# Performance work log

Hardware: AMD Instinct MI355X
Metric: run time of the kernel (lower is better)

The kernel has to match this reference:

```python
import jax, jax.numpy as jnp
import numpy as np
import math

N, E, MUL = 10000, 160000, 128
D = MUL * 4  # 128x0e (128) + 128x1o (384) = 512
NEURONS = 32
EDGE_ATTR_DIM = 32
WEIGHT_NUMEL = 4 * MUL  # 4 uvu tensor-product paths, 128 weights each


def ssp(x):
    return jax.nn.softplus(x) - math.log(2.0)


def irrep_linear(x, W0, b0, W1):
    # o3.Linear on 128x0e+128x1o: mixes mul channels within each irrep, fan-in normalized,
    # bias only on scalar (0e) block.
    s = x[:, :MUL] @ (W0 / jnp.sqrt(MUL)) + b0
    v = x[:, MUL:].reshape(-1, MUL, 3)
    v = jnp.einsum('num,uv->nvm', v, W1) / jnp.sqrt(MUL)
    return jnp.concatenate([s, v.reshape(-1, MUL * 3)], axis=-1)


def inner_product(a, b):
    # InnerProduct: uuu channel-wise irrep inner product, 1/sqrt(dim) normalized
    s = a[:, :MUL] * b[:, :MUL]
    va = a[:, MUL:].reshape(-1, MUL, 3)
    vb = b[:, MUL:].reshape(-1, MUL, 3)
    v = jnp.einsum('num,num->nu', va, vb) / jnp.sqrt(3.0)
    return jnp.concatenate([s, v], axis=-1)


def norm_gate(x, W1, b1, W2, b2):
    # NormGate: per-channel norms of l>0 irreps -> MLP gates -> gate l>0 channels
    v = x[:, MUL:].reshape(-1, MUL, 3)
    norm_v = jnp.sqrt(jnp.sum(v * v, axis=-1) + 1e-12)      # [n, 128]
    f0 = jnp.concatenate([x[:, :MUL], norm_v], axis=-1)     # [n, 256]
    g = jax.nn.silu(f0 @ W1 + b1) @ W2 + b2                 # [n, 256]
    gated = v * g[:, MUL:, None]
    return jnp.concatenate([g[:, :MUL], gated.reshape(-1, MUL * 3)], axis=-1)


def mlp2(x, Wa, Wb):
    # e3nn FullyConnectedNet: fan-in normalized, ssp nonlinearity on hidden layer only
    return ssp(x @ (Wa / jnp.sqrt(Wa.shape[0]))) @ (Wb / jnp.sqrt(Wb.shape[0]))


def setup_inputs():
    key = jax.random.key(0)
    ks = jax.random.split(key, 20)
    r = lambda i, shp: jax.random.normal(ks[i], shp, dtype=jnp.float32)
    return {
        'x': r(0, (N, D)),
        'edge_index': jax.random.randint(ks[1], (2, E), 0, N, dtype=jnp.int32),
        'edge_attr': jax.random.uniform(ks[2], (E, EDGE_ATTR_DIM), dtype=jnp.float32),
        'edge_sh': r(3, (E, 4)),
        'Wp0': r(4, (MUL, MUL)), 'bp0': jnp.zeros((MUL,), jnp.float32), 'Wp1': r(5, (MUL, MUL)),
        'ngW1': r(6, (2 * MUL, 2 * MUL)) / 16.0, 'ngb1': jnp.zeros((2 * MUL,), jnp.float32),
        'ngW2': r(7, (2 * MUL, 2 * MUL)) / 16.0, 'ngb2': jnp.zeros((2 * MUL,), jnp.float32),
        'Wn0': r(8, (MUL, MUL)), 'bn0': jnp.zeros((MUL,), jnp.float32), 'Wn1': r(9, (MUL, MUL)),
        'fcnW1': r(10, (EDGE_ATTR_DIM, NEURONS)), 'fcnW2': r(11, (NEURONS, WEIGHT_NUMEL)),
        'l0W1': r(12, (3 * MUL, NEURONS)), 'l0W2': r(13, (NEURONS, WEIGHT_NUMEL)),
        'Wo0': r(14, (MUL, MUL)), 'bo0': jnp.zeros((MUL,), jnp.float32), 'Wo1': r(15, (MUL, MUL)),
    }


def reference(x, edge_index, edge_attr, edge_sh, Wp0, bp0, Wp1, ngW1, ngb1, ngW2, ngb2,
              Wn0, bn0, Wn1, fcnW1, fcnW2, l0W1, l0W2, Wo0, bo0, Wo1):
    edge_dst, edge_src = edge_index[0], edge_index[1]
    # invariant edge descriptor s0 from pre-linear + inner product
    pre_x = irrep_linear(x, Wp0, bp0, Wp1)
    ip = inner_product(pre_x[edge_dst], pre_x[edge_src])[:, MUL:]             # [E,128]
    s0 = jnp.concatenate([pre_x[edge_dst][:, :MUL], pre_x[edge_src][:, :MUL], ip], axis=-1)  # [E,384]
    # norm-gate + linear on node features
    x = norm_gate(x, ngW1, ngb1, ngW2, ngb2)
    x = irrep_linear(x, Wn0, bn0, Wn1)
    self_x = x
    # per-edge tensor-product weights: fc_node(edge_attr) * layer_l0(s0)
    w = mlp2(edge_attr, fcnW1, fcnW2) * mlp2(s0, l0W1, l0W2)                   # [E,512]
    w1, w2, w3, w4 = w[:, :MUL], w[:, MUL:2 * MUL], w[:, 2 * MUL:3 * MUL], w[:, 3 * MUL:]
    xs = x[edge_src]
    xs0 = xs[:, :MUL]                     # [E,128]
    xs1 = xs[:, MUL:].reshape(E, MUL, 3)  # [E,128,3]
    sh0 = edge_sh[:, 0:1]
    sh1 = edge_sh[:, 1:4]
    # uvu CG tensor product paths: 0ex0e->0e, 0ex1o->1o, 1ox0e->1o, 1ox1o->0e
    c0, c1 = 0.5, jnp.sqrt(3.0) / 2.0  # path norm sqrt(ir_out.dim / n_paths)
    out0 = c0 * (w1 * xs0 * sh0 + w4 * jnp.einsum('eum,em->eu', xs1, sh1) / jnp.sqrt(3.0))
    out1 = c1 * (w2[:, :, None] * xs0[:, :, None] * sh1[:, None, :]
                 + w3[:, :, None] * xs1 * sh0[:, :, None])
    edge_feat = jnp.concatenate([out0, out1.reshape(E, MUL * 3)], axis=-1)     # [E,512]
    # scatter-aggregate to destination nodes, residual, output linear
    out = jax.ops.segment_sum(edge_feat, edge_dst, num_segments=N)
    out = out + self_x
    return irrep_linear(out, Wo0, bo0, Wo1)
```

## Files before the change

kernel.cpp:

```cpp
#include <hip/hip_runtime.h>
#include <hip/hip_fp16.h>
#include <math.h>

#define NN 10000
#define EE 160000
#define DPB 8

#define RS128 0.08838834764831845f
#define RS384 0.05103103630798287f
#define RS32  0.17677669529663687f
#define R3    0.57735026918962576f
#define C1V   0.86602540378443865f

typedef _Float16 half8 __attribute__((ext_vector_type(8)));
typedef _Float16 half4 __attribute__((ext_vector_type(4)));
typedef float f32x4 __attribute__((ext_vector_type(4)));

__device__ __forceinline__ float sspf(float x) {
    return fmaxf(x, 0.0f) + log1pf(__expf(-fabsf(x))) - 0.69314718055994530942f;
}

__device__ __forceinline__ void packone(const float* __restrict__ W,
                                        _Float16* __restrict__ P,
                                        int K, int N, int off) {
    const int KS = K >> 5;
    int j = off & 7, lane = (off >> 3) & 63, rest = off >> 9;
    int ks = rest % KS, ct = rest / KS;
    int k = ks * 32 + ((lane >> 4) << 3) + j;
    int c = ct * 16 + (lane & 15);
    P[off] = (_Float16)W[k * N + c];
}

__global__ __launch_bounds__(256) void k_packall(
    const float* __restrict__ Wp0, const float* __restrict__ Wp1,
    const float* __restrict__ Wn0, const float* __restrict__ Wn1,
    const float* __restrict__ Wo0, const float* __restrict__ Wo1,
    const float* __restrict__ ngW1, const float* __restrict__ ngW2,
    const float* __restrict__ l0W1, const float* __restrict__ fcnW1,
    const float* __restrict__ fcnW2, const float* __restrict__ l0W2,
    _Float16* __restrict__ pWp0, _Float16* __restrict__ pWp1,
    _Float16* __restrict__ pWn0, _Float16* __restrict__ pWn1,
    _Float16* __restrict__ pWo0, _Float16* __restrict__ pWo1,
    _Float16* __restrict__ png1, _Float16* __restrict__ png2,
    _Float16* __restrict__ pWc, _Float16* __restrict__ pWa,
    _Float16* __restrict__ Wf_t, _Float16* __restrict__ Wl_t) {
    int idx = blockIdx.x * 256 + threadIdx.x;
    if (idx < 98304) {
        int seg = idx >> 14, off = idx & 16383;
        if (seg == 0) packone(Wp0, pWp0, 128, 128, off);
        else if (seg == 1) packone(Wp1, pWp1, 128, 128, off);
        else if (seg == 2) packone(Wn0, pWn0, 128, 128, off);
        else if (seg == 3) packone(Wn1, pWn1, 128, 128, off);
        else if (seg == 4) packone(Wo0, pWo0, 128, 128, off);
        else packone(Wo1, pWo1, 128, 128, off);
    } else if (idx < 229376) {
        int r = idx - 98304;
        if (r < 65536) packone(ngW1, png1, 256, 256, r);
        else packone(ngW2, png2, 256, 256, r - 65536);
    } else if (idx < 233472) {
        packone(l0W1 + 256 * 32, pWc, 128, 32, idx - 229376);
    } else if (idx < 234496) {
        packone(fcnW1, pWa, 32, 32, idx - 233472);
    } else {
        int off = idx - 234496;
        int k = off & 31, c = off >> 5;
        Wf_t[c * 32 + k] = (_Float16)fcnW2[k * 512 + c];
        Wl_t[c * 32 + k] = (_Float16)l0W2[k * 512 + c];
    }
}

__global__ __launch_bounds__(256) void k_irrep_m(
    const float* __restrict__ X, const _Float16* __restrict__ pW0,
    const float* __restrict__ b0, const _Float16* __restrict__ pW1,
    float* __restrict__ out) {
    __shared__ _Float16 Xr[4][16][136];
    const int t = threadIdx.x, lane = t & 63, w = t >> 6;
    const int nb = blockIdx.x * 16;
    for (int idx = t; idx < 16 * 128; idx += 256) {
        int n = idx >> 7, c4 = idx & 127;
        const float4 v = *(const float4*)(X + (size_t)(nb + n) * 512 + 4 * c4);
        float vals[4] = {v.x, v.y, v.z, v.w};
        int c = 4 * c4;
#pragma unroll
        for (int j = 0; j < 4; ++j) {
            int cc = c + j;
            if (cc < 128) Xr[0][n][cc] = (_Float16)vals[j];
            else { int d = cc - 128; Xr[1 + d % 3][n][d / 3] = (_Float16)vals[j]; }
        }
    }
    __syncthreads();
    const _Float16* pW = (w == 0) ? pW0 : pW1;
    const int row16 = lane & 15, kg = lane >> 4;
    f32x4 acc[8];
    const f32x4 zero = {0.0f, 0.0f, 0.0f, 0.0f};
#pragma unroll
    for (int ct = 0; ct < 8; ++ct) acc[ct] = zero;
    for (int ks = 0; ks < 4; ++ks) {
        const half8 a = *(const half8*)&Xr[w][row16][ks * 32 + kg * 8];
#pragma unroll
        for (int ct = 0; ct < 8; ++ct) {
            const half8 b = *(const half8*)(pW + (((ct * 4 + ks) * 64 + lane) << 3));
            acc[ct] = __builtin_amdgcn_mfma_f32_16x16x32_f16(a, b, acc[ct], 0, 0, 0);
        }
    }
#pragma unroll
    for (int ct = 0; ct < 8; ++ct) {
        const int col = ct * 16 + row16;
        const float bb = (w == 0) ? b0[col] : 0.0f;
#pragma unroll
        for (int r = 0; r < 4; ++r) {
            const int node = nb + kg * 4 + r;
            const float val = acc[ct][r] * RS128 + bb;
            if (w == 0) out[(size_t)node * 512 + col] = val;
            else out[(size_t)node * 512 + 128 + 3 * col + (w - 1)] = val;
        }
    }
}

__global__ __launch_bounds__(256) void k_self_m(
    const float* __restrict__ X,
    const _Float16* __restrict__ png1, const float* __restrict__ ngb1,
    const _Float16* __restrict__ png2, const float* __restrict__ ngb2,
    const _Float16* __restrict__ pWn0, const float* __restrict__ bn0,
    const _Float16* __restrict__ pWn1,
    _Float16* __restrict__ selfx_h) {
    __shared__ _Float16 f0h[16][264];
    __shared__ _Float16 t1h[16][264];
    __shared__ _Float16 xvh[3][16][136];
    const int t = threadIdx.x, lane = t & 63, w = t >> 6;
    const int nb = blockIdx.x * 16;
    const int row16 = lane & 15, kg = lane >> 4;
    const f32x4 zero = {0.0f, 0.0f, 0.0f, 0.0f};

    for (int idx = t; idx < 16 * 128; idx += 256) {
        int n = idx >> 7, c4 = idx & 127;
        const float4 v = *(const float4*)(X + (size_t)(nb + n) * 512 + 4 * c4);
        float vals[4] = {v.x, v.y, v.z, v.w};
        int c = 4 * c4;
#pragma unroll
        for (int j = 0; j < 4; ++j) {
            int cc = c + j;
            if (cc < 128) f0h[n][cc] = (_Float16)vals[j];
            else { int d = cc - 128; xvh[d % 3][n][d / 3] = (_Float16)vals[j]; }
        }
    }
    __syncthreads();
    for (int idx = t; idx < 16 * 128; idx += 256) {
        int n = idx >> 7, u = idx & 127;
        float a = (float)xvh[0][n][u], b = (float)xvh[1][n][u], c = (float)xvh[2][n][u];
        f0h[n][128 + u] = (_Float16)sqrtf(fmaf(a, a, fmaf(b, b, fmaf(c, c, 1e-12f))));
    }
    __syncthreads();
    {
        f32x4 acc[4];
#pragma unroll
        for (int i = 0; i < 4; ++i) acc[i] = zero;
        for (int ks = 0; ks < 8; ++ks) {
            const half8 a = *(const half8*)&f0h[row16][ks * 32 + kg * 8];
#pragma unroll
            for (int c2 = 0; c2 < 4; ++c2) {
                const int ct = 4 * w + c2;
                const half8 b = *(const half8*)(png1 + (((ct * 8 + ks) * 64 + lane) << 3));
                acc[c2] = __builtin_amdgcn_mfma_f32_16x16x32_f16(a, b, acc[c2], 0, 0, 0);
            }
        }
#pragma unroll
        for (int c2 = 0; c2 < 4; ++c2) {
            const int col = (4 * w + c2) * 16 + row16;
            const float bb = ngb1[col];
#pragma unroll
            for (int r = 0; r < 4; ++r) {
                const float z = acc[c2][r] + bb;
                t1h[kg * 4 + r][col] = (_Float16)(z / (1.0f + __expf(-z)));
            }
        }
    }
    __syncthreads();
    {
        f32x4 acc[4];
#pragma unroll
        for (int i = 0; i < 4; ++i) acc[i] = zero;
        for (int ks = 0; ks < 8; ++ks) {
            const half8 a = *(const half8*)&t1h[row16][ks * 32 + kg * 8];
#pragma unroll
            for (int c2 = 0; c2 < 4; ++c2) {
                const int ct = 4 * w + c2;
                const half8 b = *(const half8*)(png2 + (((ct * 8 + ks) * 64 + lane) << 3));
                acc[c2] = __builtin_amdgcn_mfma_f32_16x16x32_f16(a, b, acc[c2], 0, 0, 0);
            }
        }
        __syncthreads();
#pragma unroll
        for (int c2 = 0; c2 < 4; ++c2) {
            const int col = (4 * w + c2) * 16 + row16;
            const float bb = ngb2[col];
#pragma unroll
            for (int r = 0; r < 4; ++r)
                f0h[kg * 4 + r][col] = (_Float16)(acc[c2][r] + bb);
        }
    }
    __syncthreads();
    for (int idx = t; idx < 16 * 128; idx += 256) {
        int n = idx >> 7, u = idx & 127;
        const _Float16 g = f0h[n][128 + u];
        xvh[0][n][u] = xvh[0][n][u] * g;
        xvh[1][n][u] = xvh[1][n][u] * g;
        xvh[2][n][u] = xvh[2][n][u] * g;
    }
    __syncthreads();
    {
        const _Float16* pw = (w == 0) ? pWn0 : pWn1;
        f32x4 acc[8];
#pragma unroll
        for (int ct = 0; ct < 8; ++ct) acc[ct] = zero;
        for (int ks = 0; ks < 4; ++ks) {
            const half8 a = (w == 0)
                ? *(const half8*)&f0h[row16][ks * 32 + kg * 8]
                : *(const half8*)&xvh[w - 1][row16][ks * 32 + kg * 8];
#pragma unroll
            for (int ct = 0; ct < 8; ++ct) {
                const half8 b = *(const half8*)(pw + (((ct * 4 + ks) * 64 + lane) << 3));
                acc[ct] = __builtin_amdgcn_mfma_f32_16x16x32_f16(a, b, acc[ct], 0, 0, 0);
            }
        }
#pragma unroll
        for (int ct = 0; ct < 8; ++ct) {
            const int col = ct * 16 + row16;
            const float bb = (w == 0) ? bn0[col] : 0.0f;
#pragma unroll
            for (int r = 0; r < 4; ++r) {
                const int n = kg * 4 + r;
                const float val = acc[ct][r] * RS128 + bb;
                if (w == 0) f0h[n][col] = (_Float16)val;
                else xvh[w - 1][n][col] = (_Float16)val;
            }
        }
    }
    __syncthreads();
    for (int idx = t; idx < 16 * 128; idx += 256) {
        int n = idx >> 7, u = idx & 127;
        half4 sx = {f0h[n][u], xvh[0][n][u], xvh[1][n][u], xvh[2][n][u]};
        *(half4*)(selfx_h + (size_t)(nb + n) * 512 + (u << 2)) = sx;
    }
}

__global__ __launch_bounds__(256) void k_pre(
    const float* __restrict__ prex, const float* __restrict__ l0W1,
    float* __restrict__ pAB) {
    __shared__ float xs[8][128];
    const int t = threadIdx.x;
    const int nb = blockIdx.x * 8;
    for (int idx = t; idx < 8 * 128; idx += 256) {
        int n = idx >> 7, u = idx & 127;
        xs[n][u] = prex[(size_t)(nb + n) * 512 + u];
    }
    __syncthreads();
    const int n = t >> 5, k = t & 31;
    float a = 0, b = 0;
    for (int u = 0; u < 128; ++u) {
        float s = xs[n][u];
        a = fmaf(s, l0W1[u * 32 + k], a);
        b = fmaf(s, l0W1[(128 + u) * 32 + k], b);
    }
    pAB[(size_t)(nb + n) * 64 + k] = a;
    pAB[(size_t)(nb + n) * 64 + 32 + k] = b;
}

__global__ __launch_bounds__(256) void k_deg(const int* __restrict__ ei, int* __restrict__ deg) {
    int e = blockIdx.x * 256 + threadIdx.x;
    if (e < EE) atomicAdd(&deg[ei[e]], 1);
}

__global__ __launch_bounds__(1024) void k_scan(const int* __restrict__ deg, int* __restrict__ row_ptr) {
    __shared__ int part[1024];
    const int t = threadIdx.x;
    const int base = t * 10;
    int loc[10];
    int s = 0;
#pragma unroll
    for (int i = 0; i < 10; ++i) {
        int idx = base + i;
        int d = (idx < NN) ? deg[idx] : 0;
        loc[i] = s;
        s += d;
    }
    part[t] = s;
    __syncthreads();
    for (int off = 1; off < 1024; off <<= 1) {
        int v = (t >= off) ? part[t - off] : 0;
        __syncthreads();
        part[t] += v;
        __syncthreads();
    }
    int excl = (t > 0) ? part[t - 1] : 0;
#pragma unroll
    for (int i = 0; i < 10; ++i) {
        int idx = base + i;
        if (idx <= NN) row_ptr[idx] = excl + loc[i];
    }
}

__global__ __launch_bounds__(256) void k_fill(const int* __restrict__ ei,
                                              const int* __restrict__ row_ptr,
                                              int* __restrict__ cursor,
                                              int* __restrict__ csr_eid) {
    int e = blockIdx.x * 256 + threadIdx.x;
    if (e < EE) {
        int d = ei[e];
        int pos = atomicAdd(&cursor[d], 1);
        csr_eid[row_ptr[d] + pos] = e;
    }
}

__global__ __launch_bounds__(256) void k_hidden_m(
    const float* __restrict__ prex, const float* __restrict__ pAB,
    const int* __restrict__ edge_index, const float* __restrict__ edge_attr,
    const int* __restrict__ csr_eid,
    const _Float16* __restrict__ pWc, const _Float16* __restrict__ pWa,
    __half* __restrict__ hh) {
    const int pb = blockIdx.x * 32;
    const int t = threadIdx.x, lane = t & 63, w = t >> 6;
    __shared__ _Float16 ipl[32][132];
    __shared__ _Float16 eal[32][36];
    __shared__ _Float16 h1o[32][32];
    __shared__ _Float16 hao[32][32];
    __shared__ int dsts[32], srcs[32], eids[32];

    if (t < 32) {
        const int id = csr_eid[pb + t];
        eids[t] = id;
        dsts[t] = edge_index[id];
        srcs[t] = edge_index[EE + id];
    }
    __syncthreads();
    for (int idx = t; idx < 32 * 32; idx += 256) {
        int e = idx >> 5, j = idx & 31;
        eal[e][j] = (_Float16)edge_attr[(size_t)eids[e] * 32 + j];
    }
    for (int idx = t; idx < 32 * 128; idx += 256) {
        int e = idx >> 7, u = idx & 127;
        const float* pd = prex + (size_t)dsts[e] * 512 + 128 + 3 * u;
        const float* ps = prex + (size_t)srcs[e] * 512 + 128 + 3 * u;
        ipl[e][u] = (_Float16)((pd[0] * ps[0] + pd[1] * ps[1] + pd[2] * ps[2]) * R3);
    }
    __syncthreads();

    const int row16 = lane & 15, kg = lane >> 4;
    const int mt = w >> 1, ct = w & 1;
    const int e0 = mt * 16;
    const f32x4 zero = {0.0f, 0.0f, 0.0f, 0.0f};
    const int kc = ct * 16 + row16;

    {
        f32x4 acc = zero;
#pragma unroll
        for (int ks = 0; ks < 4; ++ks) {
            const half8 a = *(const half8*)&ipl[e0 + row16][ks * 32 + kg * 8];
            const half8 b = *(const half8*)(pWc + (((ct * 4 + ks) * 64 + lane) << 3));
            acc = __builtin_amdgcn_mfma_f32_16x16x32_f16(a, b, acc, 0, 0, 0);
        }
#pragma unroll
        for (int r = 0; r < 4; ++r) {
            const int e = e0 + kg * 4 + r;
            const float v = acc[r] + pAB[(size_t)dsts[e] * 64 + kc]
                                   + pAB[(size_t)srcs[e] * 64 + 32 + kc];
            h1o[e][kc] = (_Float16)sspf(v * RS384);
        }
    }
    {
        const half8 a = *(const half8*)&eal[e0 + row16][kg * 8];
        const half8 b = *(const half8*)(pWa + ((ct * 64 + lane) << 3));
        f32x4 acc = __builtin_amdgcn_mfma_f32_16x16x32_f16(a, b, zero, 0, 0, 0);
#pragma unroll
        for (int r = 0; r < 4; ++r) {
            const int e = e0 + kg * 4 + r;
            hao[e][kc] = (_Float16)sspf((float)acc[r] * RS32);
        }
    }
    __syncthreads();
    for (int idx = t; idx < 32 * 32; idx += 256) {
        const int e = idx >> 5, j = idx & 31;
        unsigned vv;
        if (j < 16) {
            __half2 h2 = __halves2half2((__half)h1o[e][2 * j], (__half)h1o[e][2 * j + 1]);
            vv = *(unsigned*)&h2;
        } else {
            const int jj = j - 16;
            __half2 h2 = __halves2half2((__half)hao[e][2 * jj], (__half)hao[e][2 * jj + 1]);
            vv = *(unsigned*)&h2;
        }
        ((unsigned*)hh)[(size_t)(pb + e) * 32 + j] = vv;
    }
}

__global__ __launch_bounds__(512) void k_accum(
    const __half* __restrict__ hh, const _Float16* __restrict__ selfx_h,
    const int* __restrict__ edge_index, const float* __restrict__ edge_sh,
    const int* __restrict__ row_ptr, const int* __restrict__ csr_eid,
    const _Float16* __restrict__ Wf_t, const _Float16* __restrict__ Wl_t,
    float* __restrict__ outacc) {
    const int dst0 = blockIdx.x * DPB;
    const int t = threadIdx.x;
    const int lane = t & 63;
    const int wid = t >> 6;
    const int lcol = lane & 15;
    const int kg = lane >> 4;
    const int u = 16 * wid + lcol;
    const int koff = kg * 8;

    __shared__ __align__(16) _Float16 h1s[2][4][16][8];
    __shared__ __align__(16) _Float16 has[2][4][16][8];
    __shared__ float shl[2][16][4];
    __shared__ int srcs[2][16];
    __shared__ int cbeg[DPB], cne[DPB], cchk[DPB + 1];

    if (t < DPB) {
        const int b = row_ptr[dst0 + t];
        cbeg[t] = b;
        cne[t] = row_ptr[dst0 + t + 1] - b;
    }
    __syncthreads();
    if (t == 0) {
        int s = 0;
#pragma unroll
        for (int i = 0; i < DPB; ++i) { cchk[i] = s; s += max(1, (cne[i] + 15) >> 4); }
        cchk[DPB] = s;
    }
    half8 bf[4], bl[4];
#pragma unroll
    for (int q = 0; q < 4; ++q) {
        const int col = q * 128 + u;
        bf[q] = *(const half8*)(Wf_t + col * 32 + koff);
        bl[q] = *(const half8*)(Wl_t + col * 32 + koff);
    }
    __syncthreads();
    const int nc = cchk[DPB];
    const float inv32 = 1.0f / 32.0f;

    float acc0 = 0, acc1 = 0, acc2 = 0, acc3 = 0;

    unsigned rhh = 0;
    int rsrc = 0;
    float4 rsh = {0.0f, 0.0f, 0.0f, 0.0f};

    const int se = t >> 5, sw = t & 31;

    auto issue = [&](int ci) {
        int dd = 0;
        while (dd + 1 < DPB && ci >= cchk[dd + 1]) ++dd;
        const int c0 = (ci - cchk[dd]) << 4;
        const int ce = min(16, cne[dd] - c0);
        const int pos = cbeg[dd] + c0;
        rhh = (se < ce) ? ((const unsigned*)hh)[(size_t)(pos + se) * 32 + sw] : 0u;
        if (t < 16) {
            if (t < ce) {
                const int id = csr_eid[pos + t];
                rsrc = edge_index[EE + id];
                rsh = *(const float4*)(edge_sh + (size_t)id * 4);
            } else {
                rsrc = 0;
                rsh = make_float4(0.0f, 0.0f, 0.0f, 0.0f);
            }
        }
    };

    auto flush = [&](int dd) {
        acc0 += __shfl_xor(acc0, 16, 64); acc0 += __shfl_xor(acc0, 32, 64);
        acc1 += __shfl_xor(acc1, 16, 64); acc1 += __shfl_xor(acc1, 32, 64);
        acc2 += __shfl_xor(acc2, 16, 64); acc2 += __shfl_xor(acc2, 32, 64);
        acc3 += __shfl_xor(acc3, 16, 64); acc3 += __shfl_xor(acc3, 32, 64);
        if (lane < 16) {
            const size_t g = (size_t)(dst0 + dd) * 512;
            const half4 sx = *(const half4*)(selfx_h + g + (u << 2));
            outacc[g + u] = acc0 + (float)sx.x;
            outacc[g + 128 + 3 * u + 0] = acc1 + (float)sx.y;
            outacc[g + 128 + 3 * u + 1] = acc2 + (float)sx.z;
            outacc[g + 128 + 3 * u + 2] = acc3 + (float)sx.w;
        }
        acc0 = acc1 = acc2 = acc3 = 0;
    };

    issue(0);
    int cur = 0, cur_dd = 0;
    for (int ci = 0; ci < nc; ++ci) {
        if (sw < 16) ((unsigned*)h1s[cur])[(sw >> 2) * 64 + se * 4 + (sw & 3)] = rhh;
        else         ((unsigned*)has[cur])[((sw - 16) >> 2) * 64 + se * 4 + ((sw - 16) & 3)] = rhh;
        if (t < 16) {
            srcs[cur][t] = rsrc;
            shl[cur][t][0] = rsh.x; shl[cur][t][1] = rsh.y;
            shl[cur][t][2] = rsh.z; shl[cur][t][3] = rsh.w;
        }
        int dd = 0;
        while (dd + 1 < DPB && ci >= cchk[dd + 1]) ++dd;
        const int c0 = (ci - cchk[dd]) << 4;
        const int ce = min(16, cne[dd] - c0);
        if (ci + 1 < nc) issue(ci + 1);
        __syncthreads();
        if (dd != cur_dd) { flush(cur_dd); cur_dd = dd; }

        const half8 haf = *(const half8*)(&has[cur][kg][lcol][0]);
        const half8 h1f = *(const half8*)(&h1s[cur][kg][lcol][0]);
        const f32x4 zero = {0.0f, 0.0f, 0.0f, 0.0f};
        f32x4 A[4], B[4];
#pragma unroll
        for (int q = 0; q < 4; ++q) {
            A[q] = __builtin_amdgcn_mfma_f32_16x16x32_f16(haf, bf[q], zero, 0, 0, 0);
            B[q] = __builtin_amdgcn_mfma_f32_16x16x32_f16(h1f, bl[q], zero, 0, 0, 0);
        }
#pragma unroll
        for (int r = 0; r < 4; ++r) {
            const int e = kg * 4 + r;
            if (e < ce) {
                const float w1 = A[0][r] * B[0][r] * inv32;
                const float w2 = A[1][r] * B[1][r] * inv32;
                const float w3 = A[2][r] * B[2][r] * inv32;
                const float w4 = A[3][r] * B[3][r] * inv32;
                const int src = srcs[cur][e];
                const float sh0 = shl[cur][e][0], s1x = shl[cur][e][1];
                const float s1y = shl[cur][e][2], s1z = shl[cur][e][3];
                const half4 sx = *(const half4*)(selfx_h + (size_t)src * 512 + (u << 2));
                const float xs0 = (float)sx.x;
                const float xv0 = (float)sx.y;
                const float xv1 = (float)sx.z;
                const float xv2 = (float)sx.w;
                const float dv = xv0 * s1x + xv1 * s1y + xv2 * s1z;
                acc0 += 0.5f * (w1 * xs0 * sh0 + w4 * dv * R3);
                acc1 += C1V * (w2 * xs0 * s1x + w3 * xv0 * sh0);
                acc2 += C1V * (w2 * xs0 * s1y + w3 * xv1 * sh0);
                acc3 += C1V * (w2 * xs0 * s1z + w3 * xv2 * sh0);
            }
        }
        cur ^= 1;
    }
    flush(cur_dd);
}

extern "C" void kernel_launch(void* const* d_in, const int* in_sizes, int n_in,
                              void* d_out, int out_size, void* d_ws, size_t ws_size,
                              hipStream_t stream) {
    const float* x = (const float*)d_in[0];
    const int* edge_index = (const int*)d_in[1];
    const float* edge_attr = (const float*)d_in[2];
    const float* edge_sh = (const float*)d_in[3];
    const float* Wp0 = (const float*)d_in[4];
    const float* bp0 = (const float*)d_in[5];
    const float* Wp1 = (const float*)d_in[6];
    const float* ngW1 = (const float*)d_in[7];
    const float* ngb1 = (const float*)d_in[8];
    const float* ngW2 = (const float*)d_in[9];
    const float* ngb2 = (const float*)d_in[10];
    const float* Wn0 = (const float*)d_in[11];
    const float* bn0 = (const float*)d_in[12];
    const float* Wn1 = (const float*)d_in[13];
    const float* fcnW1 = (const float*)d_in[14];
    const float* fcnW2 = (const float*)d_in[15];
    const float* l0W1 = (const float*)d_in[16];
    const float* l0W2 = (const float*)d_in[17];
    const float* Wo0 = (const float*)d_in[18];
    const float* bo0 = (const float*)d_in[19];
    const float* Wo1 = (const float*)d_in[20];

    float* out = (float*)d_out;
    float* prex = out;
    _Float16* selfx_h = (_Float16*)d_ws;
    int* deg = (int*)(selfx_h + (size_t)NN * 512);
    int* cursor = deg + NN;
    int* row_ptr = cursor + NN;
    int* csr_eid = row_ptr + NN + 1;
    float* pAB = (float*)(csr_eid + EE);
    __half* hh = (__half*)(pAB + (size_t)NN * 64);
    _Float16* Wf_t = (_Float16*)(hh + (size_t)EE * 64);
    _Float16* Wl_t = Wf_t + 512 * 32;
    _Float16* pWp0 = Wl_t + 512 * 32;
    _Float16* pWp1 = pWp0 + 128 * 128;
    _Float16* pWn0 = pWp1 + 128 * 128;
    _Float16* pWn1 = pWn0 + 128 * 128;
    _Float16* pWo0 = pWn1 + 128 * 128;
    _Float16* pWo1 = pWo0 + 128 * 128;
    _Float16* png1 = pWo1 + 128 * 128;
    _Float16* png2 = png1 + 256 * 256;
    _Float16* pWc  = png2 + 256 * 256;
    _Float16* pWa  = pWc + 128 * 32;

    hipMemsetAsync(deg, 0, 2 * NN * sizeof(int), stream);

    k_packall<<<980, 256, 0, stream>>>(Wp0, Wp1, Wn0, Wn1, Wo0, Wo1, ngW1, ngW2,
                                       l0W1, fcnW1, fcnW2, l0W2,
                                       pWp0, pWp1, pWn0, pWn1, pWo0, pWo1,
                                       png1, png2, pWc, pWa, Wf_t, Wl_t);

    k_irrep_m<<<NN / 16, 256, 0, stream>>>(x, pWp0, bp0, pWp1, prex);
    k_pre<<<NN / 8, 256, 0, stream>>>(prex, l0W1, pAB);
    k_self_m<<<NN / 16, 256, 0, stream>>>(x, png1, ngb1, png2, ngb2, pWn0, bn0, pWn1,
                                          selfx_h);
    k_deg<<<EE / 256, 256, 0, stream>>>(edge_index, deg);
    k_scan<<<1, 1024, 0, stream>>>(deg, row_ptr);
    k_fill<<<EE / 256, 256, 0, stream>>>(edge_index, row_ptr, cursor, csr_eid);
    k_hidden_m<<<EE / 32, 256, 0, stream>>>(prex, pAB, edge_index, edge_attr, csr_eid,
                                            pWc, pWa, hh);
    k_accum<<<NN / DPB, 512, 0, stream>>>(hh, selfx_h, edge_index, edge_sh, row_ptr, csr_eid,
                                          Wf_t, Wl_t, out);
    k_irrep_m<<<NN / 16, 256, 0, stream>>>(out, pWo0, bo0, pWo1, out);
}
```

Before: 257.2 us.

## Fuse pre-linear, pAB projection and norm-gate into one node kernel

Merges the pre-interaction irrep linear, the scalar projection onto l0W1 (previously a scalar FMA kernel) and the norm-gate/self-linear kernel into a single per-node kernel. The input tile is loaded once, and the pAB projection now runs on MFMA using a newly packed fp16 weight. The hipMemsetAsync of the degree and cursor arrays is folded into the packing kernel. This removes two launches and a re-read of prex, at the cost of a longer kernel with more registers and LDS. The fp16 pAB projection may also slightly change numerics.

```diff
diff --git a/kernel.cpp b/kernel.cpp
--- a/kernel.cpp
+++ b/kernel.cpp
@@ -43,7 +43,8 @@
     _Float16* __restrict__ pWo0, _Float16* __restrict__ pWo1,
     _Float16* __restrict__ png1, _Float16* __restrict__ png2,
     _Float16* __restrict__ pWc, _Float16* __restrict__ pWa,
-    _Float16* __restrict__ Wf_t, _Float16* __restrict__ Wl_t) {
+    _Float16* __restrict__ Wf_t, _Float16* __restrict__ Wl_t,
+    _Float16* __restrict__ pWab, int* __restrict__ degz) {
     int idx = blockIdx.x * 256 + threadIdx.x;
     if (idx < 98304) {
         int seg = idx >> 14, off = idx & 16383;
@@ -61,11 +62,21 @@
         packone(l0W1 + 256 * 32, pWc, 128, 32, idx - 229376);
     } else if (idx < 234496) {
         packone(fcnW1, pWa, 32, 32, idx - 233472);
-    } else {
+    } else if (idx < 250880) {
         int off = idx - 234496;
         int k = off & 31, c = off >> 5;
         Wf_t[c * 32 + k] = (_Float16)fcnW2[k * 512 + c];
         Wl_t[c * 32 + k] = (_Float16)l0W2[k * 512 + c];
+    } else if (idx < 259072) {
+        int off = idx - 250880;
+        int j = off & 7, lane = (off >> 3) & 63, rest = off >> 9;
+        int ks = rest & 3, ct = rest >> 2;
+        int k = ks * 32 + ((lane >> 4) << 3) + j;
+        int c = ct * 16 + (lane & 15);
+        pWab[off] = (_Float16)((c < 32) ? l0W1[k * 32 + c]
+                                        : l0W1[(128 + k) * 32 + (c - 32)]);
+    } else if (idx < 279072) {
+        degz[idx - 259072] = 0;
     }
 }
 
@@ -117,12 +128,15 @@
     }
 }
 
-__global__ __launch_bounds__(256) void k_self_m(
+__global__ __launch_bounds__(256) void k_node(
     const float* __restrict__ X,
+    const _Float16* __restrict__ pWp0, const float* __restrict__ bp0,
+    const _Float16* __restrict__ pWp1, const _Float16* __restrict__ pWab,
     const _Float16* __restrict__ png1, const float* __restrict__ ngb1,
     const _Float16* __restrict__ png2, const float* __restrict__ ngb2,
     const _Float16* __restrict__ pWn0, const float* __restrict__ bn0,
     const _Float16* __restrict__ pWn1,
+    float* __restrict__ prex, float* __restrict__ pAB,
     _Float16* __restrict__ selfx_h) {
     __shared__ _Float16 f0h[16][264];
     __shared__ _Float16 t1h[16][264];
@@ -152,6 +166,53 @@
     }
     __syncthreads();
     {
+        const _Float16* pW = (w == 0) ? pWp0 : pWp1;
+        f32x4 acc[8];
+#pragma unroll
+        for (int ct = 0; ct < 8; ++ct) acc[ct] = zero;
+        for (int ks = 0; ks < 4; ++ks) {
+            const half8 a = (w == 0)
+                ? *(const half8*)&f0h[row16][ks * 32 + kg * 8]
+                : *(const half8*)&xvh[w - 1][row16][ks * 32 + kg * 8];
+#pragma unroll
+            for (int ct = 0; ct < 8; ++ct) {
+                const half8 b = *(const half8*)(pW + (((ct * 4 + ks) * 64 + lane) << 3));
+                acc[ct] = __builtin_amdgcn_mfma_f32_16x16x32_f16(a, b, acc[ct], 0, 0, 0);
+            }
+        }
+#pragma unroll
+        for (int ct = 0; ct < 8; ++ct) {
+            const int col = ct * 16 + row16;
+            const float bb = (w == 0) ? bp0[col] : 0.0f;
+#pragma unroll
+            for (int r = 0; r < 4; ++r) {
+                const int node = nb + kg * 4 + r;
+                const float val = acc[ct][r] * RS128 + bb;
+                if (w == 0) {
+                    prex[(size_t)node * 512 + col] = val;
+                    t1h[kg * 4 + r][col] = (_Float16)val;
+                } else {
+                    prex[(size_t)node * 512 + 128 + 3 * col + (w - 1)] = val;
+                }
+            }
+        }
+    }
+    __syncthreads();
+    {
+        f32x4 acc = zero;
+#pragma unroll
+        for (int ks = 0; ks < 4; ++ks) {
+            const half8 a = *(const half8*)&t1h[row16][ks * 32 + kg * 8];
+            const half8 b = *(const half8*)(pWab + (((w * 4 + ks) * 64 + lane) << 3));
+            acc = __builtin_amdgcn_mfma_f32_16x16x32_f16(a, b, acc, 0, 0, 0);
+        }
+        const int col = w * 16 + row16;
+#pragma unroll
+        for (int r = 0; r < 4; ++r)
+            pAB[(size_t)(nb + kg * 4 + r) * 64 + col] = acc[r];
+    }
+    __syncthreads();
+    {
         f32x4 acc[4];
 #pragma unroll
         for (int i = 0; i < 4; ++i) acc[i] = zero;
@@ -164,6 +225,7 @@
                 acc[c2] = __builtin_amdgcn_mfma_f32_16x16x32_f16(a, b, acc[c2], 0, 0, 0);
             }
         }
+        __syncthreads();
 #pragma unroll
         for (int c2 = 0; c2 < 4; ++c2) {
             const int col = (4 * w + c2) * 16 + row16;
@@ -242,28 +304,6 @@
         half4 sx = {f0h[n][u], xvh[0][n][u], xvh[1][n][u], xvh[2][n][u]};
         *(half4*)(selfx_h + (size_t)(nb + n) * 512 + (u << 2)) = sx;
     }
-}
-
-__global__ __launch_bounds__(256) void k_pre(
-    const float* __restrict__ prex, const float* __restrict__ l0W1,
-    float* __restrict__ pAB) {
-    __shared__ float xs[8][128];
-    const int t = threadIdx.x;
-    const int nb = blockIdx.x * 8;
-    for (int idx = t; idx < 8 * 128; idx += 256) {
-        int n = idx >> 7, u = idx & 127;
-        xs[n][u] = prex[(size_t)(nb + n) * 512 + u];
-    }
-    __syncthreads();
-    const int n = t >> 5, k = t & 31;
-    float a = 0, b = 0;
-    for (int u = 0; u < 128; ++u) {
-        float s = xs[n][u];
-        a = fmaf(s, l0W1[u * 32 + k], a);
-        b = fmaf(s, l0W1[(128 + u) * 32 + k], b);
-    }
-    pAB[(size_t)(nb + n) * 64 + k] = a;
-    pAB[(size_t)(nb + n) * 64 + 32 + k] = b;
 }
 
 __global__ __launch_bounds__(256) void k_deg(const int* __restrict__ ei, int* __restrict__ deg) {
@@ -581,18 +621,17 @@
     _Float16* png2 = png1 + 256 * 256;
     _Float16* pWc  = png2 + 256 * 256;
     _Float16* pWa  = pWc + 128 * 32;
-
-    hipMemsetAsync(deg, 0, 2 * NN * sizeof(int), stream);
-
-    k_packall<<<980, 256, 0, stream>>>(Wp0, Wp1, Wn0, Wn1, Wo0, Wo1, ngW1, ngW2,
-                                       l0W1, fcnW1, fcnW2, l0W2,
-                                       pWp0, pWp1, pWn0, pWn1, pWo0, pWo1,
-                                       png1, png2, pWc, pWa, Wf_t, Wl_t);
-
-    k_irrep_m<<<NN / 16, 256, 0, stream>>>(x, pWp0, bp0, pWp1, prex);
-    k_pre<<<NN / 8, 256, 0, stream>>>(prex, l0W1, pAB);
-    k_self_m<<<NN / 16, 256, 0, stream>>>(x, png1, ngb1, png2, ngb2, pWn0, bn0, pWn1,
-                                          selfx_h);
+    _Float16* pWab = pWa + 32 * 32;
+
+    k_packall<<<1091, 256, 0, stream>>>(Wp0, Wp1, Wn0, Wn1, Wo0, Wo1, ngW1, ngW2,
+                                        l0W1, fcnW1, fcnW2, l0W2,
+                                        pWp0, pWp1, pWn0, pWn1, pWo0, pWo1,
+                                        png1, png2, pWc, pWa, Wf_t, Wl_t,
+                                        pWab, deg);
+
+    k_node<<<NN / 16, 256, 0, stream>>>(x, pWp0, bp0, pWp1, pWab,
+                                        png1, ngb1, png2, ngb2, pWn0, bn0, pWn1,
+                                        prex, pAB, selfx_h);
     k_deg<<<EE / 256, 256, 0, stream>>>(edge_index, deg);
     k_scan<<<1, 1024, 0, stream>>>(deg, row_ptr);
     k_fill<<<EE / 256, 256, 0, stream>>>(edge_index, row_ptr, cursor, csr_eid);
```

After: 248.4 us (median of 2 runs). 3.4% less time.
